# Kernel optimization log

Hardware: AMD Instinct MI355X
Metric: run time of the kernel (lower is better)

The kernel has to match this reference:

```python
import jax, jax.numpy as jnp
import numpy as np

M_CH = 3        # channel index from shapelet_info['pos'][1]
DIL = 4         # dilation
EPS = 1e-8      # pDic['scale_epsilon']


def setup_inputs() -> dict:
    key = jax.random.key(0)
    k1, k2 = jax.random.split(key, 2)
    B, C, Q, L = 512, 8, 4096, 32
    W = Q - (L - 1) * DIL  # 3972
    x = jax.random.normal(k1, (B, C, Q), dtype=jnp.float32)
    shapelet = jax.random.normal(k2, (L,), dtype=jnp.float32)
    posMap = jnp.zeros((W,), dtype=jnp.float32)
    posSlope = jnp.float32(1.0)
    return {"x": x, "shapelet": shapelet, "posMap": posMap, "posSlope": posSlope, "ep": 1}


def reference(x, shapelet, posMap, posSlope, ep):
    # x: [B, C, Q]; pick channel m, dilated unfold -> [B, W, L]
    B, C, Q = x.shape
    L = shapelet.shape[0]
    W = Q - (L - 1) * DIL
    xc = x[:, M_CH, :]                                        # [B, Q]
    idx = jnp.arange(W)[:, None] + jnp.arange(L)[None, :] * DIL  # [W, L]
    xu = xc[:, idx]                                           # [B, W, L]
    # scaleType == 2: z-normalize each subsequence (torch.std is unbiased -> ddof=1)
    mean = jnp.mean(xu, axis=-1, keepdims=True)
    std = jnp.std(xu, axis=-1, ddof=1, keepdims=True)
    xu = (xu - mean) / (std + EPS)
    # squared distance, mean over L
    d = jnp.mean((shapelet[None, None, :] - xu) ** 2, axis=-1)  # [B, W]
    # positional weighting: posSlope*elu(-posMap) + 2.0
    w = posSlope * jax.nn.elu(-posMap) + 2.0                  # [W]
    ftrs = d * w[None, :]                                     # [B, W] (sum over singleton channel dim is identity)
    agg = jnp.min(ftrs, axis=-1)                              # [B]
    return jax.nn.relu(agg)[:, None]                          # [B, 1]
```

## Files before the change

kernel.cpp:

```cpp
#include <hip/hip_runtime.h>
#include <math.h>

#define M_CH 3
#define DILC 4
#define EPSC 1e-8f
#define LC   32
#define QC   4096
#define WC   3972
#define NWC  993
#define RUNC 16

__device__ __forceinline__ int skew(int a) { return a + (a >> 6); }

__global__ __launch_bounds__(256) void feature_kernel(
    const float* __restrict__ x,
    const float* __restrict__ shp,
    const float* __restrict__ posMap,
    const float* __restrict__ posSlope_p,
    float* __restrict__ out,
    int C)
{
    __shared__ float sx[4352];
    __shared__ float sw[4160];
    __shared__ float smin[4];

    const int tid = threadIdx.x;
    const int b   = blockIdx.x;
    const float* __restrict__ xr = x + ((size_t)b * C + M_CH) * QC;

    {
        const float4* xr4 = reinterpret_cast<const float4*>(xr);
        #pragma unroll
        for (int i = 0; i < QC / 4 / 256; ++i) {
            int a4 = tid + i * 256;
            float4 v = xr4[a4];
            int s = skew(a4 * 4);
            sx[s] = v.x; sx[s + 1] = v.y; sx[s + 2] = v.z; sx[s + 3] = v.w;
        }
    }
    {
        const float ps = posSlope_p[0];
        const float4* pm4 = reinterpret_cast<const float4*>(posMap);
        #pragma unroll
        for (int i = 0; i < 4; ++i) {
            int a4 = tid + i * 256;
            if (a4 < NWC) {
                float4 z = pm4[a4];
                float e0 = (-z.x > 0.f) ? -z.x : (__expf(-z.x) - 1.f);
                float e1 = (-z.y > 0.f) ? -z.y : (__expf(-z.y) - 1.f);
                float e2 = (-z.z > 0.f) ? -z.z : (__expf(-z.z) - 1.f);
                float e3 = (-z.w > 0.f) ? -z.w : (__expf(-z.w) - 1.f);
                int s = skew(a4 * 4);
                sw[s]     = fmaf(ps, e0, 2.0f);
                sw[s + 1] = fmaf(ps, e1, 2.0f);
                sw[s + 2] = fmaf(ps, e2, 2.0f);
                sw[s + 3] = fmaf(ps, e3, 2.0f);
            }
        }
    }
    __syncthreads();

    float sreg[LC];
    #pragma unroll
    for (int j = 0; j < LC; ++j) sreg[j] = shp[j];
    float Ssum = 0.f, S2 = 0.f;
    #pragma unroll
    for (int j = 0; j < LC; ++j) { Ssum += sreg[j]; S2 = fmaf(sreg[j], sreg[j], S2); }

    const int lane = tid & 63;
    const int r    = tid >> 6;
    const int w0   = 64 * lane + r;

    float buf[32];
    #pragma unroll
    for (int p = 0; p < 32; ++p) {
        int a = w0 + DILC * p;
        buf[p] = sx[skew(a)];
    }
    float sum = 0.f, sq = 0.f;
    #pragma unroll
    for (int p = 0; p < 32; ++p) { sum += buf[p]; sq = fmaf(buf[p], buf[p], sq); }

    const float invL  = 1.0f / 32.0f;
    const float invL1 = 1.0f / 31.0f;
    float best = INFINITY;

    #pragma unroll
    for (int k = 0; k < RUNC; ++k) {
        if (k > 0) {
            int slot = (k + 31) & 31;
            float oldv = buf[slot];
            int a = w0 + DILC * k + (LC - 1) * DILC;
            float newv = sx[skew(a)];
            sum += newv - oldv;
            sq  += fmaf(newv, newv, -(oldv * oldv));
            buf[slot] = newv;
        }
        float dot = 0.f;
        #pragma unroll
        for (int j = 0; j < LC; ++j)
            dot = fmaf(sreg[j], buf[(k + j) & 31], dot);

        const bool valid = (RUNC * lane + k) < NWC;
        const int  w     = w0 + DILC * k;
        float wv = sw[skew(w)];

        float m   = sum * invL;
        float var = (sq - 32.0f * m * m) * invL1;
        var = fmaxf(var, 0.0f);
        float sd  = __builtin_amdgcn_sqrtf(var) + EPSC;
        float inv = __builtin_amdgcn_rcpf(sd);
        float d = S2 * invL
                - 2.0f * (dot - m * Ssum) * invL * inv
                + (sq * invL - m * m) * inv * inv;

        float f = valid ? d * wv : INFINITY;
        best = fminf(best, f);
    }

    #pragma unroll
    for (int off = 32; off > 0; off >>= 1)
        best = fminf(best, __shfl_down(best, off, 64));
    if (lane == 0) smin[r] = best;
    __syncthreads();
    if (tid == 0) {
        float m01 = fminf(smin[0], smin[1]);
        float m23 = fminf(smin[2], smin[3]);
        out[b] = fmaxf(fminf(m01, m23), 0.0f);
    }
}

extern "C" void kernel_launch(void* const* d_in, const int* in_sizes, int n_in,
                              void* d_out, int out_size, void* d_ws, size_t ws_size,
                              hipStream_t stream) {
    const float* x        = (const float*)d_in[0];
    const float* shp      = (const float*)d_in[1];
    const float* posSlope = (const float*)d_in[3];
    const float* posMap   = (const float*)d_in[2];
    float* out = (float*)d_out;

    const int C = 8;
    const int B = in_sizes[0] / (C * QC);

    feature_kernel<<<B, 256, 0, stream>>>(x, shp, posMap, posSlope, out, C);
}
```

Before: 11.56 us.

## Split each row across two blocks, precompute position weights in an init kernel

```diff
diff --git a/kernel.cpp b/kernel.cpp
--- a/kernel.cpp
+++ b/kernel.cpp
@@ -1,61 +1,55 @@
 #include <hip/hip_runtime.h>
 #include <math.h>
 
-#define M_CH 3
 #define DILC 4
 #define EPSC 1e-8f
 #define LC   32
 #define QC   4096
 #define WC   3972
-#define NWC  993
-#define RUNC 16
+#define CBLK 1988
+#define NST4 528
+#define RUN  8
+#define NU   497
 
 __device__ __forceinline__ int skew(int a) { return a + (a >> 6); }
+
+__global__ __launch_bounds__(256) void init_kernel(
+    const float* __restrict__ posMap, const float* __restrict__ posSlope_p,
+    float* __restrict__ pw, float* __restrict__ out, int B)
+{
+    int t = blockIdx.x * 256 + threadIdx.x;
+    if (t < WC) {
+        float ps = posSlope_p[0];
+        float z = -posMap[t];
+        float e = (z > 0.f) ? z : (__expf(z) - 1.f);
+        pw[t] = fmaf(ps, e, 2.0f);
+    }
+    if (t < B) out[t] = INFINITY;
+}
 
 __global__ __launch_bounds__(256) void feature_kernel(
     const float* __restrict__ x,
     const float* __restrict__ shp,
-    const float* __restrict__ posMap,
-    const float* __restrict__ posSlope_p,
+    const float* __restrict__ pw,
     float* __restrict__ out,
     int C)
 {
-    __shared__ float sx[4352];
-    __shared__ float sw[4160];
+    __shared__ float sx[2240];
     __shared__ float smin[4];
 
     const int tid = threadIdx.x;
-    const int b   = blockIdx.x;
-    const float* __restrict__ xr = x + ((size_t)b * C + M_CH) * QC;
+    const int b   = blockIdx.x >> 1;
+    const int h   = blockIdx.x & 1;
+    const float* __restrict__ xr = x + ((size_t)b * C + 3) * QC + h * CBLK;
 
-    {
-        const float4* xr4 = reinterpret_cast<const float4*>(xr);
-        #pragma unroll
-        for (int i = 0; i < QC / 4 / 256; ++i) {
-            int a4 = tid + i * 256;
+    const float4* xr4 = reinterpret_cast<const float4*>(xr);
+    #pragma unroll
+    for (int i = 0; i < 3; ++i) {
+        int a4 = tid + i * 256;
+        if (a4 < NST4) {
             float4 v = xr4[a4];
             int s = skew(a4 * 4);
-            sx[s] = v.x; sx[s + 1] = v.y; sx[s + 2] = v.z; sx[s + 3] = v.w;
-        }
-    }
-    {
-        const float ps = posSlope_p[0];
-        const float4* pm4 = reinterpret_cast<const float4*>(posMap);
-        #pragma unroll
-        for (int i = 0; i < 4; ++i) {
-            int a4 = tid + i * 256;
-            if (a4 < NWC) {
-                float4 z = pm4[a4];
-                float e0 = (-z.x > 0.f) ? -z.x : (__expf(-z.x) - 1.f);
-                float e1 = (-z.y > 0.f) ? -z.y : (__expf(-z.y) - 1.f);
-                float e2 = (-z.z > 0.f) ? -z.z : (__expf(-z.z) - 1.f);
-                float e3 = (-z.w > 0.f) ? -z.w : (__expf(-z.w) - 1.f);
-                int s = skew(a4 * 4);
-                sw[s]     = fmaf(ps, e0, 2.0f);
-                sw[s + 1] = fmaf(ps, e1, 2.0f);
-                sw[s + 2] = fmaf(ps, e2, 2.0f);
-                sw[s + 3] = fmaf(ps, e3, 2.0f);
-            }
+            sx[s] = v.x; sx[s+1] = v.y; sx[s+2] = v.z; sx[s+3] = v.w;
         }
     }
     __syncthreads();
@@ -69,41 +63,53 @@
 
     const int lane = tid & 63;
     const int r    = tid >> 6;
-    const int w0   = 64 * lane + r;
+    const int u0   = RUN * lane;
 
     float buf[32];
     #pragma unroll
-    for (int p = 0; p < 32; ++p) {
-        int a = w0 + DILC * p;
-        buf[p] = sx[skew(a)];
+    for (int p = 0; p < 32; ++p)
+        buf[p] = sx[skew(r + 4 * (u0 + p))];
+
+    float a0=0,a1=0,a2=0,a3=0, q0=0,q1=0,q2=0,q3=0;
+    #pragma unroll
+    for (int p = 0; p < 32; p += 4) {
+        a0 += buf[p];   q0 = fmaf(buf[p],   buf[p],   q0);
+        a1 += buf[p+1]; q1 = fmaf(buf[p+1], buf[p+1], q1);
+        a2 += buf[p+2]; q2 = fmaf(buf[p+2], buf[p+2], q2);
+        a3 += buf[p+3]; q3 = fmaf(buf[p+3], buf[p+3], q3);
     }
-    float sum = 0.f, sq = 0.f;
-    #pragma unroll
-    for (int p = 0; p < 32; ++p) { sum += buf[p]; sq = fmaf(buf[p], buf[p], sq); }
+    float sum = (a0+a1)+(a2+a3);
+    float sq  = (q0+q1)+(q2+q3);
 
     const float invL  = 1.0f / 32.0f;
     const float invL1 = 1.0f / 31.0f;
     float best = INFINITY;
 
     #pragma unroll
-    for (int k = 0; k < RUNC; ++k) {
+    for (int k = 0; k < RUN; ++k) {
         if (k > 0) {
             int slot = (k + 31) & 31;
             float oldv = buf[slot];
-            int a = w0 + DILC * k + (LC - 1) * DILC;
-            float newv = sx[skew(a)];
+            float newv = sx[skew(r + 4 * (u0 + k + 31))];
             sum += newv - oldv;
             sq  += fmaf(newv, newv, -(oldv * oldv));
             buf[slot] = newv;
         }
-        float dot = 0.f;
+        float d0=0,d1=0,d2=0,d3=0;
         #pragma unroll
-        for (int j = 0; j < LC; ++j)
-            dot = fmaf(sreg[j], buf[(k + j) & 31], dot);
+        for (int j = 0; j < LC; j += 4) {
+            d0 = fmaf(sreg[j],   buf[(k+j)   & 31], d0);
+            d1 = fmaf(sreg[j+1], buf[(k+j+1) & 31], d1);
+            d2 = fmaf(sreg[j+2], buf[(k+j+2) & 31], d2);
+            d3 = fmaf(sreg[j+3], buf[(k+j+3) & 31], d3);
+        }
+        float dot = (d0+d1)+(d2+d3);
 
-        const bool valid = (RUNC * lane + k) < NWC;
-        const int  w     = w0 + DILC * k;
-        float wv = sw[skew(w)];
+        int  u     = u0 + k;
+        int  w     = h * CBLK + r + 4 * u;
+        bool valid = (u < NU) && (w < WC);
+        int  wi    = (w < WC) ? w : (WC - 1);
+        float wv   = pw[wi];
 
         float m   = sum * invL;
         float var = (sq - 32.0f * m * m) * invL1;
@@ -126,7 +132,8 @@
     if (tid == 0) {
         float m01 = fminf(smin[0], smin[1]);
         float m23 = fminf(smin[2], smin[3]);
-        out[b] = fmaxf(fminf(m01, m23), 0.0f);
+        float bm  = fmaxf(fminf(m01, m23), 0.0f);
+        atomicMin(reinterpret_cast<unsigned int*>(out) + b, __float_as_uint(bm));
     }
 }
 
@@ -135,12 +142,14 @@
                               hipStream_t stream) {
     const float* x        = (const float*)d_in[0];
     const float* shp      = (const float*)d_in[1];
+    const float* posMap   = (const float*)d_in[2];
     const float* posSlope = (const float*)d_in[3];
-    const float* posMap   = (const float*)d_in[2];
     float* out = (float*)d_out;
+    float* pw  = (float*)d_ws;
 
     const int C = 8;
     const int B = in_sizes[0] / (C * QC);
 
-    feature_kernel<<<B, 256, 0, stream>>>(x, shp, posMap, posSlope, out, C);
+    init_kernel<<<(WC + 255) / 256, 256, 0, stream>>>(posMap, posSlope, pw, out, B);
+    feature_kernel<<<B * 2, 256, 0, stream>>>(x, shp, pw, out, C);
 }
```

Result: slower. 16.63 us (+43.8%).
